# Kernel optimization log

Measured on AMD Instinct MI355X. Metric: run time of the kernel, lower is better.

## Reference

```python
import jax, jax.numpy as jnp
import numpy as np

# static 3D multi-scale configuration (transoar-style)
SS = np.array([[24, 24, 24], [12, 12, 12], [6, 6, 6], [3, 3, 3]], dtype=np.int64)  # (D,H,W) per level
NPL = SS.prod(1)
LSI = np.concatenate([[0], np.cumsum(NPL)[:-1]]).astype(np.int64)
S = int(NPL.sum())  # 15795 flattened tokens
B, C, HH, L, P = 2, 256, 8, 4, 4
DH = C // HH
NQ, FF = 80, 1024
NENC, NDEC = 6, 6
EPS = 1e-5


def layer_norm(x, g, b):
    mu = jnp.mean(x, -1, keepdims=True)
    var = jnp.mean((x - mu) ** 2, -1, keepdims=True)
    return (x - mu) * jax.lax.rsqrt(var + EPS) * g + b


def mha(q, k, v, in_w, in_b, out_w, out_b, mask=None):
    # torch nn.MultiheadAttention math (batch-first layout here)
    wq, wk, wv = jnp.split(in_w, 3, 0)
    bq, bk, bv = jnp.split(in_b, 3, 0)
    qh = (q @ wq.T + bq).reshape(B, -1, HH, DH)
    kh = (k @ wk.T + bk).reshape(B, -1, HH, DH)
    vh = (v @ wv.T + bv).reshape(B, -1, HH, DH)
    logits = jnp.einsum('bqhd,bkhd->bhqk', qh, kh) / jnp.float32(np.sqrt(DH))
    if mask is not None:  # bool mask, True = blocked
        logits = jnp.where(mask[None, None], jnp.float32(-1e9), logits)
    att = jax.nn.softmax(logits, -1)
    o = jnp.einsum('bhqk,bkhd->bqhd', att, vh).reshape(B, -1, C)
    return o @ out_w.T + out_b


def ms_deform_attn(query, ref, value_in, off_w, off_b, aw_w, aw_b, val_w, val_b, out_w, out_b):
    # 3D multi-scale deformable attention (deformable-DETR, trilinear sampling,
    # zero padding outside, align_corners=False semantics)
    Nq = query.shape[1]
    value = (value_in @ val_w.T + val_b).reshape(B, S, HH, DH)
    off = (query @ off_w.T + off_b).reshape(B, Nq, HH, L, P, 3)
    aw = jax.nn.softmax((query @ aw_w.T + aw_b).reshape(B, Nq, HH, L * P), -1)
    aw = aw.reshape(B, Nq, HH, L, P)
    norm = jnp.asarray(SS[:, ::-1].copy(), jnp.float32)  # (W,H,D) per level -> xyz order
    loc = ref[:, :, None, :, None, :] + off / norm[None, None, None, :, None, :]  # [B,Nq,HH,L,P,3]
    out = jnp.zeros((B, Nq, HH, DH), query.dtype)
    for lvl in range(L):
        D_, H_, W_ = (int(s) for s in SS[lvl])
        s0 = int(LSI[lvl])
        v = value[:, s0:s0 + D_ * H_ * W_].transpose(0, 2, 1, 3).reshape(B * HH, D_ * H_ * W_, DH)
        l = loc[:, :, :, lvl].transpose(0, 2, 1, 3, 4).reshape(B * HH, Nq * P, 3)
        x = l[..., 0] * W_ - 0.5
        y = l[..., 1] * H_ - 0.5
        z = l[..., 2] * D_ - 0.5
        x0, y0, z0 = jnp.floor(x), jnp.floor(y), jnp.floor(z)
        samp = jnp.zeros((B * HH, Nq * P, DH), query.dtype)
        for dz in (0, 1):
            for dy in (0, 1):
                for dx in (0, 1):
                    xi, yi, zi = x0 + dx, y0 + dy, z0 + dz
                    w = (1 - jnp.abs(x - xi)) * (1 - jnp.abs(y - yi)) * (1 - jnp.abs(z - zi))
                    ok = (xi >= 0) & (xi < W_) & (yi >= 0) & (yi < H_) & (zi >= 0) & (zi < D_)
                    idx = ((jnp.clip(zi, 0, D_ - 1) * H_ + jnp.clip(yi, 0, H_ - 1)) * W_
                           + jnp.clip(xi, 0, W_ - 1)).astype(jnp.int32)
                    samp = samp + jnp.take_along_axis(v, idx[..., None], axis=1) * (w * ok)[..., None]
        samp = samp.reshape(B, HH, Nq, P, DH)
        out = out + jnp.einsum('bhqpd,bhqp->bqhd', samp, aw[:, :, :, lvl].transpose(0, 2, 1, 3))
    return out.reshape(B, Nq, C) @ out_w.T + out_b


def get_reference_points(valid_ratios):
    refs = []
    for D_, H_, W_ in SS:
        z = (np.arange(D_) + 0.5) / D_
        y = (np.arange(H_) + 0.5) / H_
        x = (np.arange(W_) + 0.5) / W_
        zz, yy, xx = np.meshgrid(z, y, x, indexing='ij')
        refs.append(np.stack([xx.ravel(), yy.ravel(), zz.ravel()], -1))
    ref = jnp.asarray(np.concatenate(refs, 0).astype(np.float32))  # [S,3] xyz
    return ref[None, :, None, :] * valid_ratios[:, None]  # [B,S,L,3]


def _forward(fl, attn_mask):
    (src, pos, lvl_pos, tgt, query_pos, valid_ratios,
     eow, eob, eaw, eab, evw, evb, eouw, eoub, el1g, el1b, ef1w, ef1b, ef2w, ef2b, el2g, el2b,
     dsiw, dsib, dsow, dsob, dciw, dcib, dcow, dcob,
     dl1g, dl1b, dl2g, dl2b, dl3g, dl3b, df1w, df1b, df2w, df2b) = fl
    ref = get_reference_points(valid_ratios)
    out = src
    for i in range(NENC):
        a = ms_deform_attn(out + pos, ref, out, eow[i], eob[i], eaw[i], eab[i],
                           evw[i], evb[i], eouw[i], eoub[i])
        out = layer_norm(out + a, el1g[i], el1b[i])
        h = jax.nn.relu(out @ ef1w[i].T + ef1b[i])
        out = layer_norm(out + h @ ef2w[i].T + ef2b[i], el2g[i], el2b[i])
    memory = out
    q = tgt
    for i in range(NDEC):
        qk = q + query_pos
        sa = mha(qk, qk, q, dsiw[i], dsib[i], dsow[i], dsob[i])
        q = layer_norm(q + sa, dl2g[i], dl2b[i])
        ca = mha(q + query_pos, memory + lvl_pos, memory, dciw[i], dcib[i], dcow[i], dcob[i],
                 mask=attn_mask)
        q = layer_norm(q + ca, dl1g[i], dl1b[i])
        h = jax.nn.relu(q @ df1w[i].T + df1b[i])
        q = layer_norm(q + h @ df2w[i].T + df2b[i], dl3g[i], dl3b[i])
    return q


def setup_inputs() -> dict:
    key = jax.random.key(0)
    it = iter(jax.random.split(key, 64))
    def nrm(shape, s=0.02):
        return jax.random.normal(next(it), shape, jnp.float32) * s
    HLPO, HLP = HH * L * P * 3, HH * L * P
    inp = {}
    inp['src'] = nrm((B, S, C), 1.0)
    inp['pos'] = nrm((B, S, C), 1.0)
    inp['lvl_pos'] = nrm((B, S, C), 1.0)
    inp['tgt'] = nrm((B, NQ, C), 1.0)
    inp['query_pos'] = nrm((B, NQ, C), 1.0)
    inp['valid_ratios'] = jnp.ones((B, L, 3), jnp.float32)
    inp['enc_off_w'] = nrm((NENC, HLPO, C))
    inp['enc_off_b'] = nrm((NENC, HLPO), 0.1)
    inp['enc_aw_w'] = nrm((NENC, HLP, C))
    inp['enc_aw_b'] = jnp.zeros((NENC, HLP), jnp.float32)
    inp['enc_val_w'] = nrm((NENC, C, C))
    inp['enc_val_b'] = jnp.zeros((NENC, C), jnp.float32)
    inp['enc_out_w'] = nrm((NENC, C, C))
    inp['enc_out_b'] = jnp.zeros((NENC, C), jnp.float32)
    inp['enc_ln1_g'] = jnp.ones((NENC, C), jnp.float32)
    inp['enc_ln1_b'] = jnp.zeros((NENC, C), jnp.float32)
    inp['enc_fc1_w'] = nrm((NENC, FF, C))
    inp['enc_fc1_b'] = jnp.zeros((NENC, FF), jnp.float32)
    inp['enc_fc2_w'] = nrm((NENC, C, FF))
    inp['enc_fc2_b'] = jnp.zeros((NENC, C), jnp.float32)
    inp['enc_ln2_g'] = jnp.ones((NENC, C), jnp.float32)
    inp['enc_ln2_b'] = jnp.zeros((NENC, C), jnp.float32)
    inp['dec_sa_in_w'] = nrm((NDEC, 3 * C, C))
    inp['dec_sa_in_b'] = jnp.zeros((NDEC, 3 * C), jnp.float32)
    inp['dec_sa_out_w'] = nrm((NDEC, C, C))
    inp['dec_sa_out_b'] = jnp.zeros((NDEC, C), jnp.float32)
    inp['dec_ca_in_w'] = nrm((NDEC, 3 * C, C))
    inp['dec_ca_in_b'] = jnp.zeros((NDEC, 3 * C), jnp.float32)
    inp['dec_ca_out_w'] = nrm((NDEC, C, C))
    inp['dec_ca_out_b'] = jnp.zeros((NDEC, C), jnp.float32)
    inp['dec_ln1_g'] = jnp.ones((NDEC, C), jnp.float32)
    inp['dec_ln1_b'] = jnp.zeros((NDEC, C), jnp.float32)
    inp['dec_ln2_g'] = jnp.ones((NDEC, C), jnp.float32)
    inp['dec_ln2_b'] = jnp.zeros((NDEC, C), jnp.float32)
    inp['dec_ln3_g'] = jnp.ones((NDEC, C), jnp.float32)
    inp['dec_ln3_b'] = jnp.zeros((NDEC, C), jnp.float32)
    inp['dec_fc1_w'] = nrm((NDEC, FF, C))
    inp['dec_fc1_b'] = jnp.zeros((NDEC, FF), jnp.float32)
    inp['dec_fc2_w'] = nrm((NDEC, C, FF))
    inp['dec_fc2_b'] = jnp.zeros((NDEC, C), jnp.float32)
    inp['attn_mask'] = jax.random.bernoulli(next(it), 0.5, (NQ, S))
    inp['spatial_shapes'] = jnp.asarray(SS, jnp.int32)
    inp['level_start_index'] = jnp.asarray(LSI, jnp.int32)
    return inp


def reference(src, pos, lvl_pos, tgt, query_pos, valid_ratios,
              enc_off_w, enc_off_b, enc_aw_w, enc_aw_b, enc_val_w, enc_val_b, enc_out_w, enc_out_b,
              enc_ln1_g, enc_ln1_b, enc_fc1_w, enc_fc1_b, enc_fc2_w, enc_fc2_b, enc_ln2_g, enc_ln2_b,
              dec_sa_in_w, dec_sa_in_b, dec_sa_out_w, dec_sa_out_b,
              dec_ca_in_w, dec_ca_in_b, dec_ca_out_w, dec_ca_out_b,
              dec_ln1_g, dec_ln1_b, dec_ln2_g, dec_ln2_b, dec_ln3_g, dec_ln3_b,
              dec_fc1_w, dec_fc1_b, dec_fc2_w, dec_fc2_b,
              attn_mask, spatial_shapes, level_start_index):
    fl = (src, pos, lvl_pos, tgt, query_pos, valid_ratios,
          enc_off_w, enc_off_b, enc_aw_w, enc_aw_b, enc_val_w, enc_val_b, enc_out_w, enc_out_b,
          enc_ln1_g, enc_ln1_b, enc_fc1_w, enc_fc1_b, enc_fc2_w, enc_fc2_b, enc_ln2_g, enc_ln2_b,
          dec_sa_in_w, dec_sa_in_b, dec_sa_out_w, dec_sa_out_b,
          dec_ca_in_w, dec_ca_in_b, dec_ca_out_w, dec_ca_out_b,
          dec_ln1_g, dec_ln1_b, dec_ln2_g, dec_ln2_b, dec_ln3_g, dec_ln3_b,
          dec_fc1_w, dec_fc1_b, dec_fc2_w, dec_fc2_b)
    return _forward(fl, attn_mask)
```

## Files before the change

### kernel.cpp

```cpp
#include <hip/hip_runtime.h>
#include <cstdint>

#define S_TOT 15795
#define B_SZ 2
#define NQ 80
#define XSPLIT 128
#define NSPLIT 124
#define XCHUNK 128
#define MP 31616

typedef __attribute__((ext_vector_type(8))) short short8;
typedef __attribute__((ext_vector_type(4))) float f32x4;
typedef __attribute__((ext_vector_type(2))) float f32x2;

__device__ __forceinline__ unsigned short f2bf(float f) {
    unsigned u = __float_as_uint(f);
    unsigned r = u + 0x7fffu + ((u >> 16) & 1u);
    return (unsigned short)(r >> 16);
}

__global__ __launch_bounds__(256)
void cast_bf16_kernel(const float* __restrict__ x, unsigned short* __restrict__ o, int n4)
{
    int i = blockIdx.x * 256 + threadIdx.x;
    if (i < n4) {
        float4 v = ((const float4*)x)[i];
        ushort4 r;
        r.x = f2bf(v.x); r.y = f2bf(v.y); r.z = f2bf(v.z); r.w = f2bf(v.w);
        ((ushort4*)o)[i] = r;
    }
}

__global__ __launch_bounds__(256)
void init_enc_kernel(const float* __restrict__ src, const float* __restrict__ pos,
                     float* __restrict__ f_out, unsigned short* __restrict__ b_out,
                     unsigned short* __restrict__ b_mlp, int n4)
{
    int i = blockIdx.x * 256 + threadIdx.x;
    if (i < n4) {
        float4 s = ((const float4*)src)[i];
        float4 p = ((const float4*)pos)[i];
        ((float4*)f_out)[i] = s;
        ushort4 r, m;
        r.x = f2bf(s.x); r.y = f2bf(s.y); r.z = f2bf(s.z); r.w = f2bf(s.w);
        m.x = f2bf(s.x + p.x); m.y = f2bf(s.y + p.y);
        m.z = f2bf(s.z + p.z); m.w = f2bf(s.w + p.w);
        ((ushort4*)b_out)[i] = r;
        ((ushort4*)b_mlp)[i] = m;
    }
}

__global__ __launch_bounds__(256)
void cast_fuse_w_kernel(const float* __restrict__ eow, const float* __restrict__ eaw,
                        unsigned short* __restrict__ o)
{
    int i = blockIdx.x * 256 + threadIdx.x;
    const int n4 = 6 * 512 * 256 / 4;
    if (i < n4) {
        int e = i * 4;
        int layer = e / (512 * 256);
        int rem = e - layer * 512 * 256;
        int row = rem >> 8, col = rem & 255;
        const float* src = (row < 384)
            ? eow + ((size_t)layer * 384 + row) * 256 + col
            : eaw + ((size_t)layer * 128 + (row - 384)) * 256 + col;
        float4 v = *(const float4*)src;
        ushort4 r;
        r.x = f2bf(v.x); r.y = f2bf(v.y); r.z = f2bf(v.z); r.w = f2bf(v.w);
        ((ushort4*)o)[i] = r;
    }
}

__global__ __launch_bounds__(512)
void fuse_bias_kernel(const float* __restrict__ eob, const float* __restrict__ eab,
                      float* __restrict__ o)
{
    int i = blockIdx.x, t = threadIdx.x;
    o[i * 512 + t] = (t < 384) ? eob[i * 384 + t] : eab[i * 128 + (t - 384)];
}

__global__ __launch_bounds__(256)
void mask_pack_kernel(const unsigned char* __restrict__ mask,
                      unsigned long long* __restrict__ mp, int Lk)
{
    __shared__ unsigned char ml[80][260];
    const int k0 = blockIdx.x * 256;
    const int t = threadIdx.x;
    for (int idx = t; idx < 80 * 256; idx += 256) {
        int q = idx >> 8, kk = idx & 255;
        int kg = k0 + kk;
        ml[q][kk] = (kg < Lk) ? mask[(size_t)q * Lk + kg] : 1;
    }
    __syncthreads();
    int kg = k0 + t;
    if (kg < Lk) {
        unsigned long long lo = 0, hi = 0;
        #pragma unroll
        for (int q = 0; q < 64; ++q)
            lo |= (unsigned long long)(ml[q][t] ? 1u : 0u) << q;
        #pragma unroll
        for (int q = 0; q < 16; ++q)
            hi |= (unsigned long long)(ml[64 + q][t] ? 1u : 0u) << q;
        mp[2 * kg] = lo; mp[2 * kg + 1] = hi;
    }
}

__global__ __launch_bounds__(256)
void gemm_bf16_kernel(const unsigned short* __restrict__ A,
                      const unsigned short* __restrict__ B,
                      const float* __restrict__ bias, void* __restrict__ Yv,
                      int M, int N, int K, int mode)
{
    __shared__ unsigned short As[2][128 * 32];
    __shared__ unsigned short Bs[2][128 * 32];
    const int t = threadIdx.x;
    const int wave = t >> 6, lane = t & 63;
    const int quad = lane >> 4, l16 = lane & 15;
    const int bm0 = blockIdx.y * 128;
    const int bn0 = blockIdx.x * 128;
    const int wm = (wave & 1) * 64;
    const int wn = (wave >> 1) * 64;
    const int srow = t >> 2;
    const int scol = (t & 3) * 8;

    f32x4 acc[4][4] = {};

    const unsigned short* pa0 = A + (size_t)(bm0 + srow) * K + scol;
    const unsigned short* pa1 = pa0 + (size_t)64 * K;
    const unsigned short* pb0 = B + (size_t)(bn0 + srow) * K + scol;
    const unsigned short* pb1 = pb0 + (size_t)64 * K;

    #define GLL(src, dst)                                                        \
        __builtin_amdgcn_global_load_lds(                                        \
            (const __attribute__((address_space(1))) unsigned int*)(const void*)(src), \
            (__attribute__((address_space(3))) unsigned int*)(void*)(dst),       \
            16, 0, 0)

    const int nk = K / 32;
    GLL(pa0, &As[0][wave * 512]);
    GLL(pa1, &As[0][2048 + wave * 512]);
    GLL(pb0, &Bs[0][wave * 512]);
    GLL(pb1, &Bs[0][2048 + wave * 512]);
    __syncthreads();

    for (int kb = 0; kb < nk; ++kb) {
        const int cur = kb & 1, nxt = cur ^ 1;
        if (kb + 1 < nk) {
            const int k0 = (kb + 1) * 32;
            GLL(pa0 + k0, &As[nxt][wave * 512]);
            GLL(pa1 + k0, &As[nxt][2048 + wave * 512]);
            GLL(pb0 + k0, &Bs[nxt][wave * 512]);
            GLL(pb1 + k0, &Bs[nxt][2048 + wave * 512]);
        }

        short8 af[4], bf[4];
        #pragma unroll
        for (int im = 0; im < 4; ++im)
            af[im] = *(const short8*)&As[cur][(wm + im * 16 + l16) * 32 + quad * 8];
        #pragma unroll
        for (int in = 0; in < 4; ++in)
            bf[in] = *(const short8*)&Bs[cur][(wn + in * 16 + l16) * 32 + quad * 8];
        #pragma unroll
        for (int im = 0; im < 4; ++im)
            #pragma unroll
            for (int in = 0; in < 4; ++in)
                acc[im][in] = __builtin_amdgcn_mfma_f32_16x16x32_bf16(
                    bf[in], af[im], acc[im][in], 0, 0, 0);

        __syncthreads();
    }
    #undef GLL

    #pragma unroll
    for (int im = 0; im < 4; ++im) {
        const int gm = bm0 + wm + im * 16 + l16;
        if (gm >= M) continue;
        #pragma unroll
        for (int in = 0; in < 4; ++in) {
            const int gn0 = bn0 + wn + in * 16 + quad * 4;
            const float4 bv = *(const float4*)(bias + gn0);
            float o0 = acc[im][in][0] + bv.x;
            float o1 = acc[im][in][1] + bv.y;
            float o2 = acc[im][in][2] + bv.z;
            float o3 = acc[im][in][3] + bv.w;
            if (mode == 1) {
                o0 = fmaxf(o0, 0.f); o1 = fmaxf(o1, 0.f);
                o2 = fmaxf(o2, 0.f); o3 = fmaxf(o3, 0.f);
            }
            if (mode == 0) {
                float4 o = make_float4(o0, o1, o2, o3);
                *(float4*)((float*)Yv + (size_t)gm * N + gn0) = o;
            } else {
                ushort4 r4;
                r4.x = f2bf(o0); r4.y = f2bf(o1);
                r4.z = f2bf(o2); r4.w = f2bf(o3);
                *(ushort4*)((unsigned short*)Yv + (size_t)gm * N + gn0) = r4;
            }
        }
    }
}

__global__ __launch_bounds__(256)
void gemm_bias_kernel(const float* __restrict__ X, const float* __restrict__ Xadd,
                      const float* __restrict__ W,
                      const float* __restrict__ bias, float* __restrict__ Y,
                      int M, int N, int K, int relu)
{
    __shared__ float Xs[16][68];
    __shared__ float Ws[16][68];
    const int bm0 = blockIdx.y * 64;
    const int bn0 = blockIdx.x * 64;
    const int t = threadIdx.x;
    const int tx = t & 15, ty = t >> 4;
    const int lr = t >> 2;
    const int lk = (t & 3) << 2;
    float acc[4][4] = {};
    const int xr = bm0 + lr;
    const int wr = bn0 + lr;
    const float* xp = X + (size_t)xr * K + lk;
    const float* xap = Xadd ? Xadd + (size_t)xr * K + lk : nullptr;
    const float* wp = W + (size_t)wr * K + lk;
    for (int k0 = 0; k0 < K; k0 += 16) {
        float4 xv = make_float4(0.f, 0.f, 0.f, 0.f);
        if (xr < M) {
            xv = *(const float4*)(xp + k0);
            if (xap) {
                float4 av = *(const float4*)(xap + k0);
                xv.x += av.x; xv.y += av.y; xv.z += av.z; xv.w += av.w;
            }
        }
        float4 wv = make_float4(0.f, 0.f, 0.f, 0.f);
        if (wr < N) wv = *(const float4*)(wp + k0);
        Xs[lk + 0][lr] = xv.x; Xs[lk + 1][lr] = xv.y;
        Xs[lk + 2][lr] = xv.z; Xs[lk + 3][lr] = xv.w;
        Ws[lk + 0][lr] = wv.x; Ws[lk + 1][lr] = wv.y;
        Ws[lk + 2][lr] = wv.z; Ws[lk + 3][lr] = wv.w;
        __syncthreads();
        #pragma unroll
        for (int k = 0; k < 16; ++k) {
            float a0 = Xs[k][ty * 4 + 0], a1 = Xs[k][ty * 4 + 1];
            float a2 = Xs[k][ty * 4 + 2], a3 = Xs[k][ty * 4 + 3];
            float b0 = Ws[k][tx * 4 + 0], b1 = Ws[k][tx * 4 + 1];
            float b2 = Ws[k][tx * 4 + 2], b3 = Ws[k][tx * 4 + 3];
            acc[0][0] += a0 * b0; acc[0][1] += a0 * b1; acc[0][2] += a0 * b2; acc[0][3] += a0 * b3;
            acc[1][0] += a1 * b0; acc[1][1] += a1 * b1; acc[1][2] += a1 * b2; acc[1][3] += a1 * b3;
            acc[2][0] += a2 * b0; acc[2][1] += a2 * b1; acc[2][2] += a2 * b2; acc[2][3] += a2 * b3;
            acc[3][0] += a3 * b0; acc[3][1] += a3 * b1; acc[3][2] += a3 * b2; acc[3][3] += a3 * b3;
        }
        __syncthreads();
    }
    const int c0 = bn0 + tx * 4;
    float4 bv = *(const float4*)(bias + c0);
    #pragma unroll
    for (int i = 0; i < 4; ++i) {
        int r = bm0 + ty * 4 + i;
        if (r >= M) continue;
        float4 o;
        o.x = acc[i][0] + bv.x; o.y = acc[i][1] + bv.y;
        o.z = acc[i][2] + bv.z; o.w = acc[i][3] + bv.w;
        if (relu) {
            o.x = fmaxf(o.x, 0.f); o.y = fmaxf(o.y, 0.f);
            o.z = fmaxf(o.z, 0.f); o.w = fmaxf(o.w, 0.f);
        }
        *(float4*)(Y + (size_t)r * N + c0) = o;
    }
}

__global__ __launch_bounds__(256)
void ln_res_kernel(const float* __restrict__ X, const float* __restrict__ R,
                   const float* __restrict__ g, const float* __restrict__ bta,
                   float* __restrict__ O, unsigned short* __restrict__ Ob,
                   const float* __restrict__ Padd, unsigned short* __restrict__ Oadd,
                   int nrows)
{
    const int row = blockIdx.x * 4 + (threadIdx.x >> 6);
    if (row >= nrows) return;
    const int t = threadIdx.x & 63;
    const float4 xv = ((const float4*)(X + (size_t)row * 256))[t];
    const float4 rv = ((const float4*)(R + (size_t)row * 256))[t];
    float v0 = xv.x + rv.x, v1 = xv.y + rv.y, v2 = xv.z + rv.z, v3 = xv.w + rv.w;
    float s = v0 + v1 + v2 + v3;
    #pragma unroll
    for (int off = 32; off >= 1; off >>= 1) s += __shfl_xor(s, off, 64);
    float mu = s * (1.f / 256.f);
    float d0 = v0 - mu, d1 = v1 - mu, d2 = v2 - mu, d3 = v3 - mu;
    float s2 = d0 * d0 + d1 * d1 + d2 * d2 + d3 * d3;
    #pragma unroll
    for (int off = 32; off >= 1; off >>= 1) s2 += __shfl_xor(s2, off, 64);
    float rstd = rsqrtf(s2 * (1.f / 256.f) + 1e-5f);
    const float4 gv = ((const float4*)g)[t];
    const float4 bv = ((const float4*)bta)[t];
    float o0 = d0 * rstd * gv.x + bv.x;
    float o1 = d1 * rstd * gv.y + bv.y;
    float o2 = d2 * rstd * gv.z + bv.z;
    float o3 = d3 * rstd * gv.w + bv.w;
    ((float4*)(O + (size_t)row * 256))[t] = make_float4(o0, o1, o2, o3);
    if (Ob) {
        ushort4 r4;
        r4.x = f2bf(o0); r4.y = f2bf(o1); r4.z = f2bf(o2); r4.w = f2bf(o3);
        ((ushort4*)(Ob + (size_t)row * 256))[t] = r4;
    }
    if (Oadd) {
        const float4 pv = ((const float4*)(Padd + (size_t)row * 256))[t];
        ushort4 r4;
        r4.x = f2bf(o0 + pv.x); r4.y = f2bf(o1 + pv.y);
        r4.z = f2bf(o2 + pv.z); r4.w = f2bf(o3 + pv.w);
        ((ushort4*)(Oadd + (size_t)row * 256))[t] = r4;
    }
}

__global__ __launch_bounds__(256)
void deform_kernel(const float* __restrict__ offaw,
                   const unsigned short* __restrict__ value,
                   unsigned short* __restrict__ out)
{
    const int nwg = B_SZ * S_TOT;
    const int qq = nwg >> 3, rr = nwg & 7;
    const int xcd = blockIdx.x & 7, chunk_off = blockIdx.x >> 3;
    const int bq = (xcd < rr ? xcd * (qq + 1) : rr * (qq + 1) + (xcd - rr) * qq) + chunk_off;
    const int b = bq / S_TOT;
    const int s = bq - b * S_TOT;
    const int t = threadIdx.x;

    __shared__ float2 tbl[128][9];

    if (t < 128) {
        const int h = t >> 4, lp = t & 15, l = lp >> 2;
        float logit = offaw[(size_t)bq * 512 + 384 + t];
        float m = logit;
        m = fmaxf(m, __shfl_xor(m, 1, 64));
        m = fmaxf(m, __shfl_xor(m, 2, 64));
        m = fmaxf(m, __shfl_xor(m, 4, 64));
        m = fmaxf(m, __shfl_xor(m, 8, 64));
        float e = __expf(logit - m);
        float su = e;
        su += __shfl_xor(su, 1, 64);
        su += __shfl_xor(su, 2, 64);
        su += __shfl_xor(su, 4, 64);
        su += __shfl_xor(su, 8, 64);
        float aw = e / su;

        int iz, iy, ix; float invn;
        if (s < 13824)      { invn = 1.f / 24.f; int tl = s;
                              iz = tl / 576; int r1 = tl - iz * 576;
                              iy = r1 / 24;  ix = r1 - iy * 24; }
        else if (s < 15552) { invn = 1.f / 12.f; int tl = s - 13824;
                              iz = tl / 144; int r1 = tl - iz * 144;
                              iy = r1 / 12;  ix = r1 - iy * 12; }
        else if (s < 15768) { invn = 1.f / 6.f;  int tl = s - 15552;
                              iz = tl / 36;  int r1 = tl - iz * 36;
                              iy = r1 / 6;   ix = r1 - iy * 6; }
        else                { invn = 1.f / 3.f;  int tl = s - 15768;
                              iz = tl / 9;   int r1 = tl - iz * 9;
                              iy = r1 / 3;   ix = r1 - iy * 3; }
        float rx = (ix + 0.5f) * invn;
        float ry = (iy + 0.5f) * invn;
        float rz = (iz + 0.5f) * invn;

        const int lvl_n[4]  = {24, 12, 6, 3};
        const int lvl_s0[4] = {0, 13824, 15552, 15768};
        const int nl = lvl_n[l];
        const int s0l = lvl_s0[l];
        const float* op = offaw + (size_t)bq * 512 + t * 3;
        float x = rx * nl + op[0] - 0.5f;
        float y = ry * nl + op[1] - 0.5f;
        float z = rz * nl + op[2] - 0.5f;
        float fx = floorf(x), fy = floorf(y), fz = floorf(z);
        int x0 = (int)fx, y0 = (int)fy, z0 = (int)fz;
        float wx1 = x - fx, wx0 = 1.f - wx1;
        float wy1 = y - fy, wy0 = 1.f - wy1;
        float wz1 = z - fz, wz0 = 1.f - wz1;
        int xc0 = min(max(x0, 0), nl - 1), xc1 = min(max(x0 + 1, 0), nl - 1);
        int yc0 = min(max(y0, 0), nl - 1), yc1 = min(max(y0 + 1, 0), nl - 1);
        int zc0 = min(max(z0, 0), nl - 1), zc1 = min(max(z0 + 1, 0), nl - 1);
        bool ox0 = (x0 >= 0) && (x0 < nl);
        bool ox1 = (x0 + 1 >= 0) && (x0 + 1 < nl);
        bool oy0 = (y0 >= 0) && (y0 < nl), oy1 = (y0 + 1 >= 0) && (y0 + 1 < nl);
        bool oz0 = (z0 >= 0) && (z0 < nl), oz1 = (z0 + 1 >= 0) && (z0 + 1 < nl);
        int base = b * S_TOT + s0l;
        #pragma unroll
        for (int c = 0; c < 8; ++c) {
            int dx = c & 1, dy = (c >> 1) & 1, dz = c >> 2;
            float w = (dx ? wx1 : wx0) * (dy ? wy1 : wy0) * (dz ? wz1 : wz0);
            bool ok = (dx ? ox1 : ox0) && (dy ? oy1 : oy0) && (dz ? oz1 : oz0);
            int xi = dx ? xc1 : xc0;
            int yi = dy ? yc1 : yc0;
            int zi = dz ? zc1 : zc0;
            int elem = ((base + (zi * nl + yi) * nl + xi) * 8 + h) << 6;
            tbl[t][c] = make_float2(ok ? w * aw : 0.f, __int_as_float(elem));
        }
    }
    __syncthreads();

    const int c16 = t & 3, z = t >> 2, cr = z & 7, h = z >> 3;
    const float2* trow = &tbl[h * 16][cr];
    const unsigned cofs = (unsigned)(c16 * 16);
    f32x2 a01 = {0.f, 0.f}, a23 = {0.f, 0.f}, a45 = {0.f, 0.f}, a67 = {0.f, 0.f};
    #pragma unroll
    for (int p = 0; p < 16; ++p) {
        float2 e = trow[p * 9];
        unsigned off = __float_as_uint(e.y) + cofs;
        const uint4 dv = *(const uint4*)((const char*)value + off);
        f32x2 w2 = {e.x, e.x};
        f32x2 v01 = {__uint_as_float(dv.x << 16), __uint_as_float(dv.x & 0xffff0000u)};
        f32x2 v23 = {__uint_as_float(dv.y << 16), __uint_as_float(dv.y & 0xffff0000u)};
        f32x2 v45 = {__uint_as_float(dv.z << 16), __uint_as_float(dv.z & 0xffff0000u)};
        f32x2 v67 = {__uint_as_float(dv.w << 16), __uint_as_float(dv.w & 0xffff0000u)};
        asm("v_pk_fma_f32 %0, %1, %2, %0" : "+v"(a01) : "v"(v01), "v"(w2));
        asm("v_pk_fma_f32 %0, %1, %2, %0" : "+v"(a23) : "v"(v23), "v"(w2));
        asm("v_pk_fma_f32 %0, %1, %2, %0" : "+v"(a45) : "v"(v45), "v"(w2));
        asm("v_pk_fma_f32 %0, %1, %2, %0" : "+v"(a67) : "v"(v67), "v"(w2));
    }
    float acc[8] = {a01.x, a01.y, a23.x, a23.y, a45.x, a45.y, a67.x, a67.y};
    #pragma unroll
    for (int i = 0; i < 8; ++i) {
        acc[i] += __shfl_xor(acc[i], 4, 64);
        acc[i] += __shfl_xor(acc[i], 8, 64);
        acc[i] += __shfl_xor(acc[i], 16, 64);
    }
    if ((t & 28) == 0) {
        uint4 r;
        r.x = (unsigned)f2bf(acc[0]) | ((unsigned)f2bf(acc[1]) << 16);
        r.y = (unsigned)f2bf(acc[2]) | ((unsigned)f2bf(acc[3]) << 16);
        r.z = (unsigned)f2bf(acc[4]) | ((unsigned)f2bf(acc[5]) << 16);
        r.w = (unsigned)f2bf(acc[6]) | ((unsigned)f2bf(acc[7]) << 16);
        *(uint4*)(out + (size_t)bq * 256 + h * 32 + c16 * 8) = r;
    }
}

__global__ __launch_bounds__(256)
void attn_kernel(const float* __restrict__ Q, const float* __restrict__ K,
                 const float* __restrict__ V, float* __restrict__ O,
                 int Lq, int Lk, float scale, int ldq, int ldk)
{
    const int nqc = (Lq + 3) >> 2;
    const int blk = blockIdx.x;
    const int qc = blk % nqc;
    const int bh = blk / nqc;
    const int h = bh & 7;
    const int b = bh >> 3;
    const int qi0 = qc * 4;
    const int t = threadIdx.x;
    const int c = t & 31, g = t >> 5;

    float qv[4];
    #pragma unroll
    for (int j = 0; j < 4; ++j)
        qv[j] = Q[((size_t)(b * Lq + qi0 + j)) * ldq + h * 32 + c];

    float m[4], l[4], acc[4];
    #pragma unroll
    for (int j = 0; j < 4; ++j) { m[j] = -1e30f; l[j] = 0.f; acc[j] = 0.f; }

    for (int k = g; k < Lk; k += 8) {
        float kv = K[((size_t)(b * Lk + k)) * ldk + h * 32 + c];
        float vv = V[((size_t)(b * Lk + k)) * 256 + h * 32 + c];
        #pragma unroll
        for (int j = 0; j < 4; ++j) {
            float p = qv[j] * kv;
            p += __shfl_xor(p, 16, 32);
            p += __shfl_xor(p, 8, 32);
            p += __shfl_xor(p, 4, 32);
            p += __shfl_xor(p, 2, 32);
            p += __shfl_xor(p, 1, 32);
            float sc = p * scale;
            float mn = fmaxf(m[j], sc);
            float fo = __expf(m[j] - mn);
            float w = __expf(sc - mn);
            l[j] = l[j] * fo + w;
            acc[j] = acc[j] * fo + w * vv;
            m[j] = mn;
        }
    }
    __shared__ float sm[8][4], sl[8][4], sacc[8][4][32];
    if (c == 0) {
        #pragma unroll
        for (int j = 0; j < 4; ++j) { sm[g][j] = m[j]; sl[g][j] = l[j]; }
    }
    #pragma unroll
    for (int j = 0; j < 4; ++j) sacc[g][j][c] = acc[j];
    __syncthreads();
    if (g == 0) {
        #pragma unroll
        for (int j = 0; j < 4; ++j) {
            float M = -1e30f;
            #pragma unroll
            for (int i = 0; i < 8; ++i) M = fmaxf(M, sm[i][j]);
            float L = 0.f, o = 0.f;
            #pragma unroll
            for (int i = 0; i < 8; ++i) {
                float e = __expf(sm[i][j] - M);
                L += sl[i][j] * e;
                o += sacc[i][j][c] * e;
            }
            O[((size_t)(b * Lq + qi0 + j)) * 256 + h * 32 + c] = o / L;
        }
    }
}

__global__ __launch_bounds__(320)
void xattn_part_kernel(const float* __restrict__ Q,
                       const unsigned short* __restrict__ K,
                       const unsigned short* __restrict__ V,
                       const unsigned long long* __restrict__ mp,
                       float* __restrict__ pm, float* __restrict__ pl,
                       float* __restrict__ po, int Lk, float scale)
{
    const int split = blockIdx.x;
    const int bh = blockIdx.y;
    const int b = bh >> 3, h = bh & 7;
    const int t = threadIdx.x;
    const int wave = t >> 6, lane = t & 63;
    const int l16 = lane & 15, quad = lane >> 4;

    __shared__ unsigned short Ks[128][40];
    __shared__ unsigned short Vt[32][136];
    __shared__ unsigned short Ps[80][40];
    __shared__ unsigned long long Mw[2][128];

    const int k_base = split * XCHUNK;

    for (int idx = t; idx < 512; idx += 320) {
        int key = idx >> 2, cg = (idx & 3) * 8;
        int kg = k_base + key;
        short8 kv = {0, 0, 0, 0, 0, 0, 0, 0};
        short8 vv = {0, 0, 0, 0, 0, 0, 0, 0};
        if (kg < Lk) {
            size_t go = ((size_t)(b * Lk + kg)) * 256 + h * 32 + cg;
            kv = *(const short8*)(K + go);
            vv = *(const short8*)(V + go);
        }
        *(short8*)&Ks[key][cg] = kv;
        #pragma unroll
        for (int j = 0; j < 8; ++j)
            Vt[cg + j][key] = (unsigned short)vv[j];
    }
    if (t < 128) {
        int kg = k_base + t;
        unsigned long long lo = ~0ULL, hi = ~0ULL;
        if (kg < Lk) { lo = mp[2 * kg]; hi = mp[2 * kg + 1]; }
        Mw[0][t] = lo; Mw[1][t] = hi;
    }

    const int q = wave * 16 + l16;
    short8 qf;
    {
        const float* qp = Q + ((size_t)(b * NQ + q)) * 256 + h * 32 + quad * 8;
        float4 q0 = *(const float4*)qp;
        float4 q1 = *(const float4*)(qp + 4);
        unsigned short* qh = (unsigned short*)&qf;
        qh[0] = f2bf(q0.x * scale); qh[1] = f2bf(q0.y * scale);
        qh[2] = f2bf(q0.z * scale); qh[3] = f2bf(q0.w * scale);
        qh[4] = f2bf(q1.x * scale); qh[5] = f2bf(q1.y * scale);
        qh[6] = f2bf(q1.z * scale); qh[7] = f2bf(q1.w * scale);
    }
    __syncthreads();

    f32x4 sfr[8];
    const f32x4 zz = {0.f, 0.f, 0.f, 0.f};
    #pragma unroll
    for (int tt = 0; tt < 8; ++tt) {
        short8 kf = *(const short8*)&Ks[tt * 16 + l16][quad * 8];
        sfr[tt] = __builtin_amdgcn_mfma_f32_16x16x32_bf16(kf, qf, zz, 0, 0, 0);
    }

    const unsigned long long* mrow = Mw[wave >> 2];
    const int qbit = (wave < 4 ? wave * 16 : 0) + l16;
    const int widx = qbit >> 5;
    const int sh = qbit & 31;

    float sc[8][4];
    #pragma unroll
    for (int tt = 0; tt < 8; ++tt) {
        int k0 = tt * 16 + quad * 4;
        uint4 ma = *(const uint4*)&mrow[k0];
        uint4 mb = *(const uint4*)&mrow[k0 + 2];
        unsigned w0 = widx ? ma.y : ma.x;
        unsigned w1 = widx ? ma.w : ma.z;
        unsigned w2 = widx ? mb.y : mb.x;
        unsigned w3 = widx ? mb.w : mb.z;
        sc[tt][0] = ((w0 >> sh) & 1u) ? -1e9f : sfr[tt][0];
        sc[tt][1] = ((w1 >> sh) & 1u) ? -1e9f : sfr[tt][1];
        sc[tt][2] = ((w2 >> sh) & 1u) ? -1e9f : sfr[tt][2];
        sc[tt][3] = ((w3 >> sh) & 1u) ? -1e9f : sfr[tt][3];
    }
    float mx = -1e30f;
    #pragma unroll
    for (int tt = 0; tt < 8; ++tt)
        #pragma unroll
        for (int r = 0; r < 4; ++r) mx = fmaxf(mx, sc[tt][r]);
    mx = fmaxf(mx, __shfl_xor(mx, 16, 64));
    mx = fmaxf(mx, __shfl_xor(mx, 32, 64));
    float sum = 0.f;
    #pragma unroll
    for (int tt = 0; tt < 8; ++tt)
        #pragma unroll
        for (int r = 0; r < 4; ++r) {
            sc[tt][r] = __expf(sc[tt][r] - mx);
            sum += sc[tt][r];
        }
    sum += __shfl_xor(sum, 16, 64);
    sum += __shfl_xor(sum, 32, 64);

    f32x4 oacc[2] = {zz, zz};
    #pragma unroll
    for (int s = 0; s < 4; ++s) {
        #pragma unroll
        for (int tt = 0; tt < 2; ++tt) {
            int T = s * 2 + tt;
            unsigned plo = (unsigned)f2bf(sc[T][0]) | ((unsigned)f2bf(sc[T][1]) << 16);
            unsigned phi = (unsigned)f2bf(sc[T][2]) | ((unsigned)f2bf(sc[T][3]) << 16);
            unsigned* dst = (unsigned*)&Ps[q][tt * 16 + quad * 4];
            dst[0] = plo; dst[1] = phi;
        }
        asm volatile("" ::: "memory");
        short8 pf = *(const short8*)&Ps[q][quad * 8];
        short8 vf0 = *(const short8*)&Vt[l16][s * 32 + quad * 8];
        short8 vf1 = *(const short8*)&Vt[16 + l16][s * 32 + quad * 8];
        oacc[0] = __builtin_amdgcn_mfma_f32_16x16x32_bf16(vf0, pf, oacc[0], 0, 0, 0);
        oacc[1] = __builtin_amdgcn_mfma_f32_16x16x32_bf16(vf1, pf, oacc[1], 0, 0, 0);
    }

    const size_t obase = ((size_t)bh * NSPLIT + split) * NQ;
    #pragma unroll
    for (int c = 0; c < 2; ++c)
        #pragma unroll
        for (int r = 0; r < 4; ++r)
            po[(obase + q) * 32 + c * 16 + quad * 4 + r] = oacc[c][r];
    if (quad == 0) { pm[obase + q] = mx; pl[obase + q] = sum; }
}

__global__ __launch_bounds__(64)
void xattn_merge_kernel(const float* __restrict__ pm, const float* __restrict__ pl,
                        const float* __restrict__ po, float* __restrict__ O)
{
    const int idx = blockIdx.x;
    const int bh = idx / NQ, q = idx - bh * NQ;
    const int b = bh >> 3, h = bh & 7;
    const int tt = threadIdx.x;
    if (tt >= 32) return;
    const int c = tt;
    float M = -1e30f;
    for (int s = 0; s < NSPLIT; ++s)
        M = fmaxf(M, pm[((size_t)bh * NSPLIT + s) * NQ + q]);
    float L = 0.f, o = 0.f;
    for (int s = 0; s < NSPLIT; ++s) {
        size_t base = ((size_t)bh * NSPLIT + s) * NQ + q;
        float e = __expf(pm[base] - M);
        L += pl[base] * e;
        o += po[base * 32 + c] * e;
    }
    O[((size_t)(b * NQ + q)) * 256 + h * 32 + c] = o / L;
}

extern "C" void kernel_launch(void* const* d_in, const int* in_sizes, int n_in,
                              void* d_out, int out_size, void* d_ws, size_t ws_size,
                              hipStream_t stream)
{
    const float* src       = (const float*)d_in[0];
    const float* pos       = (const float*)d_in[1];
    const float* lvl_pos   = (const float*)d_in[2];
    const float* tgt       = (const float*)d_in[3];
    const float* query_pos = (const float*)d_in[4];
    const float* eow  = (const float*)d_in[6];
    const float* eob  = (const float*)d_in[7];
    const float* eaw  = (const float*)d_in[8];
    const float* eab  = (const float*)d_in[9];
    const float* evw  = (const float*)d_in[10];
    const float* evb  = (const float*)d_in[11];
    const float* eouw = (const float*)d_in[12];
    const float* eoub = (const float*)d_in[13];
    const float* el1g = (const float*)d_in[14];
    const float* el1b = (const float*)d_in[15];
    const float* ef1w = (const float*)d_in[16];
    const float* ef1b = (const float*)d_in[17];
    const float* ef2w = (const float*)d_in[18];
    const float* ef2b = (const float*)d_in[19];
    const float* el2g = (const float*)d_in[20];
    const float* el2b = (const float*)d_in[21];
    const float* dsiw = (const float*)d_in[22];
    const float* dsib = (const float*)d_in[23];
    const float* dsow = (const float*)d_in[24];
    const float* dsob = (const float*)d_in[25];
    const float* dciw = (const float*)d_in[26];
    const float* dcib = (const float*)d_in[27];
    const float* dcow = (const float*)d_in[28];
    const float* dcob = (const float*)d_in[29];
    const float* dl1g = (const float*)d_in[30];
    const float* dl1b = (const float*)d_in[31];
    const float* dl2g = (const float*)d_in[32];
    const float* dl2b = (const float*)d_in[33];
    const float* dl3g = (const float*)d_in[34];
    const float* dl3b = (const float*)d_in[35];
    const float* df1w = (const float*)d_in[36];
    const float* df1b = (const float*)d_in[37];
    const float* df2w = (const float*)d_in[38];
    const float* df2b = (const float*)d_in[39];
    const unsigned char* amask = (const unsigned char*)d_in[40];

    const int MBS = B_SZ * S_TOT;
    const size_t nBSC = (size_t)MBS * 256;
    const size_t nP   = (size_t)MP * 256;
    const size_t nFFA = (size_t)MBS * 512 + 16384;

    float* ws = (float*)d_ws;
    float* f_out = ws; ws += nP;
    float* f_mlp = ws; ws += nP;
    float* f_ffa = ws; ws += nFFA;
    float* f_offaw = f_ffa;
    float* f_val = ws; ws += nP;
    float* d_q   = ws; ws += 40960;
    float* d_qkp = ws; ws += 81920;
    float* d_sq  = ws; ws += 40960;
    float* d_sv  = ws; ws += 40960;
    float* d_ao  = ws; ws += 40960;
    float* d_pr  = ws; ws += 40960;
    float* d_h   = ws; ws += 163840;
    float* x_pm  = ws; ws += (size_t)16 * XSPLIT * NQ;
    float* x_pl  = ws; ws += (size_t)16 * XSPLIT * NQ;
    float* x_po  = ws; ws += (size_t)16 * XSPLIT * NQ * 32;
    unsigned long long* x_mp = (unsigned long long*)ws; ws += 2 * 16384;
    float* f_fb  = ws; ws += 6 * 512;

    unsigned short* bws = (unsigned short*)ws;
    unsigned short* b_mlp  = bws; bws += nP;
    unsigned short* b_out  = bws; bws += nP;
    unsigned short* w_eoaw = bws; bws += (size_t)6 * 512 * 256;
    unsigned short* w_evw  = bws; bws += (size_t)6 * 256 * 256;
    unsigned short* w_eouw = bws; bws += (size_t)6 * 256 * 256;
    unsigned short* w_ef1  = bws; bws += (size_t)6 * 1024 * 256;
    unsigned short* w_ef2  = bws; bws += (size_t)6 * 256 * 1024;
    unsigned short* w_dciw = bws; bws += (size_t)6 * 768 * 256;

    unsigned short* b_hs   = (unsigned short*)f_ffa;
    unsigned short* b_samp = b_mlp;
    unsigned short* b_val  = (unsigned short*)x_pm;
    unsigned short* b_xk   = (unsigned short*)f_offaw;
    unsigned short* b_xv   = (unsigned short*)f_val;

    auto gemmb = [&](const unsigned short* A, const unsigned short* W, const float* bb,
                     void* Y, int M, int N, int K, int mode) {
        dim3 grid(N / 128, (M + 127) / 128);
        gemm_bf16_kernel<<<grid, dim3(256), 0, stream>>>(A, W, bb, Y, M, N, K, mode);
    };
    auto gemms = [&](const float* X, const float* Xadd, const float* W, const float* bb,
                     float* Y, int M, int N, int K, int relu) {
        dim3 grid(N / 64, (M + 63) / 64);
        gemm_bias_kernel<<<grid, dim3(256), 0, stream>>>(X, Xadd, W, bb, Y, M, N, K, relu);
    };
    auto cast = [&](const float* x, unsigned short* o, size_t n) {
        int n4c = (int)(n / 4);
        cast_bf16_kernel<<<(n4c + 255) / 256, 256, 0, stream>>>(x, o, n4c);
    };

    const int n4 = (int)(nBSC / 4);
    const float scale = 0.17677669529663687f;
    const int lnGrid = (MBS + 3) / 4;

    {
        const int nf4 = 6 * 512 * 256 / 4;
        cast_fuse_w_kernel<<<(nf4 + 255) / 256, 256, 0, stream>>>(eow, eaw, w_eoaw);
        fuse_bias_kernel<<<6, 512, 0, stream>>>(eob, eab, f_fb);
        mask_pack_kernel<<<(S_TOT + 255) / 256, 256, 0, stream>>>(amask, x_mp, S_TOT);
    }
    cast(evw,  w_evw,  (size_t)6 * 256 * 256);
    cast(eouw, w_eouw, (size_t)6 * 256 * 256);
    cast(ef1w, w_ef1,  (size_t)6 * 1024 * 256);
    cast(ef2w, w_ef2,  (size_t)6 * 256 * 1024);
    cast(dciw, w_dciw, (size_t)6 * 768 * 256);

    init_enc_kernel<<<(n4 + 255) / 256, 256, 0, stream>>>(src, pos, f_out, b_out, b_mlp, n4);

    for (int i = 0; i < 6; ++i) {
        gemmb(b_mlp, w_eoaw + (size_t)i * 512 * 256, f_fb + i * 512, f_offaw, MBS, 512, 256, 0);
        gemmb(b_out, w_evw + (size_t)i * 256 * 256, evb + i * 256, b_val, MBS, 256, 256, 2);
        deform_kernel<<<MBS, 256, 0, stream>>>(f_offaw, b_val, b_samp);
        gemmb(b_samp, w_eouw + (size_t)i * 256 * 256, eoub + i * 256, f_mlp, MBS, 256, 256, 0);
        ln_res_kernel<<<lnGrid, 256, 0, stream>>>(f_out, f_mlp, el1g + i * 256, el1b + i * 256,
                                                  f_out, b_out, (const float*)nullptr,
                                                  (unsigned short*)nullptr, MBS);
        gemmb(b_out, w_ef1 + (size_t)i * 1024 * 256, ef1b + i * 1024, b_hs, MBS, 1024, 256, 1);
        gemmb(b_hs, w_ef2 + (size_t)i * 256 * 1024, ef2b + i * 256, f_val, MBS, 256, 1024, 0);
        ln_res_kernel<<<lnGrid, 256, 0, stream>>>(f_out, f_val, el2g + i * 256, el2b + i * 256,
                                                  f_out, b_out, (i < 5 ? pos : lvl_pos),
                                                  b_mlp, MBS);
    }

    hipMemcpyAsync(d_q, tgt, 40960 * sizeof(float), hipMemcpyDeviceToDevice, stream);

    for (int i = 0; i < 6; ++i) {
        const float* siw = dsiw + (size_t)i * 768 * 256;
        const float* sib = dsib + (size_t)i * 768;
        gemms(d_q, query_pos, siw, sib, d_qkp, 160, 512, 256, 0);
        gemms(d_q, nullptr, siw + 512 * 256, sib + 512, d_sv, 160, 256, 256, 0);
        attn_kernel<<<B_SZ * 8 * (NQ / 4), 256, 0, stream>>>(
            d_qkp, d_qkp + 256, d_sv, d_ao, NQ, NQ, scale, 512, 512);
        gemms(d_ao, nullptr, dsow + (size_t)i * 256 * 256, dsob + i * 256, d_pr, 160, 256, 256, 0);
        ln_res_kernel<<<40, 256, 0, stream>>>(d_q, d_pr, dl2g + i * 256, dl2b + i * 256,
                                              d_q, (unsigned short*)nullptr,
                                              (const float*)nullptr, (unsigned short*)nullptr, 160);

        const float* cib = dcib + (size_t)i * 768;
        gemms(d_q, query_pos, dciw + (size_t)i * 768 * 256, cib, d_sq, 160, 256, 256, 0);
        gemmb(b_mlp, w_dciw + (size_t)i * 768 * 256 + 256 * 256, cib + 256,
              b_xk, MBS, 256, 256, 2);
        gemmb(b_out, w_dciw + (size_t)i * 768 * 256 + 512 * 256, cib + 512,
              b_xv, MBS, 256, 256, 2);
        xattn_part_kernel<<<dim3(NSPLIT, 16), 320, 0, stream>>>(
            d_sq, b_xk, b_xv, x_mp, x_pm, x_pl, x_po, S_TOT, scale);
        xattn_merge_kernel<<<16 * NQ, 64, 0, stream>>>(x_pm, x_pl, x_po, d_ao);
        gemms(d_ao, nullptr, dcow + (size_t)i * 256 * 256, dcob + i * 256, d_pr, 160, 256, 256, 0);
        ln_res_kernel<<<40, 256, 0, stream>>>(d_q, d_pr, dl1g + i * 256, dl1b + i * 256,
                                              d_q, (unsigned short*)nullptr,
                                              (const float*)nullptr, (unsigned short*)nullptr, 160);

        gemms(d_q, nullptr, df1w + (size_t)i * 1024 * 256, df1b + i * 1024, d_h, 160, 1024, 256, 1);
        gemms(d_h, nullptr, df2w + (size_t)i * 256 * 1024, df2b + i * 256, d_pr, 160, 256, 1024, 0);
        ln_res_kernel<<<40, 256, 0, stream>>>(d_q, d_pr, dl3g + i * 256, dl3b + i * 256,
                                              d_q, (unsigned short*)nullptr,
                                              (const float*)nullptr, (unsigned short*)nullptr, 160);
    }

    hipMemcpyAsync(d_out, d_q, 40960 * sizeof(float), hipMemcpyDeviceToDevice, stream);
}
```

Measured before the change: 3.709 ms.

## Fuse encoder output projections with residual add and LayerNorm in one GEMM kernel

Adds a bf16 MFMA GEMM kernel where each block computes full 256-wide rows (64 rows per block), then adds bias and the residual and applies LayerNorm in registers. It writes fp32 and bf16 outputs and, optionally, a bf16 copy with the positional embedding added. This replaces the separate out-proj/FFN2 GEMMs and ln_res kernels in the encoder, removing an fp32 intermediate round trip through memory and extra launches. The trade-off is a smaller grid (M/64 blocks) and 64 accumulator vectors per thread, which may lower occupancy for the K=1024 FFN GEMM.

Measured after the change: 3.653 ms. Within noise of the previous version (-1.5%).

```diff
diff --git a/kernel.cpp b/kernel.cpp
--- a/kernel.cpp
+++ b/kernel.cpp
@@ -196,6 +196,114 @@
                 r4.z = f2bf(o2); r4.w = f2bf(o3);
                 *(ushort4*)((unsigned short*)Yv + (size_t)gm * N + gn0) = r4;
             }
+        }
+    }
+}
+
+__global__ __launch_bounds__(256)
+void gemm_ln_kernel(const unsigned short* __restrict__ A,
+                    const unsigned short* __restrict__ B,
+                    const float* __restrict__ bias,
+                    const float* __restrict__ g, const float* __restrict__ bta,
+                    float* __restrict__ Fout, unsigned short* __restrict__ Bout,
+                    const float* __restrict__ Padd, unsigned short* __restrict__ Oadd,
+                    int M, int K)
+{
+    __shared__ unsigned short As[2][64 * 32];
+    __shared__ unsigned short Bs[2][256 * 32];
+    const int t = threadIdx.x;
+    const int wave = t >> 6, lane = t & 63;
+    const int quad = lane >> 4, l16 = lane & 15;
+    const int bm0 = blockIdx.x * 64;
+
+    f32x4 acc[16] = {};
+
+    const int srow4 = lane >> 2;
+    const int scol = (lane & 3) * 8;
+    const unsigned short* pa = A + (size_t)(bm0 + wave * 16 + srow4) * K + scol;
+    const unsigned short* pb = B + (size_t)(wave * 64 + srow4) * K + scol;
+
+    #define GLL(src, dst)                                                        \
+        __builtin_amdgcn_global_load_lds(                                        \
+            (const __attribute__((address_space(1))) unsigned int*)(const void*)(src), \
+            (__attribute__((address_space(3))) unsigned int*)(void*)(dst),       \
+            16, 0, 0)
+
+    const int nk = K / 32;
+    GLL(pa, (char*)As[0] + wave * 1024);
+    #pragma unroll
+    for (int j = 0; j < 4; ++j)
+        GLL(pb + (size_t)j * 16 * K, (char*)Bs[0] + (wave * 4 + j) * 1024);
+    __syncthreads();
+
+    for (int kb = 0; kb < nk; ++kb) {
+        const int cur = kb & 1, nxt = cur ^ 1;
+        if (kb + 1 < nk) {
+            const int k0 = (kb + 1) * 32;
+            GLL(pa + k0, (char*)As[nxt] + wave * 1024);
+            #pragma unroll
+            for (int j = 0; j < 4; ++j)
+                GLL(pb + (size_t)j * 16 * K + k0, (char*)Bs[nxt] + (wave * 4 + j) * 1024);
+        }
+
+        short8 af = *(const short8*)&As[cur][(wave * 16 + l16) * 32 + quad * 8];
+        #pragma unroll
+        for (int in = 0; in < 16; ++in) {
+            short8 bf = *(const short8*)&Bs[cur][(in * 16 + l16) * 32 + quad * 8];
+            acc[in] = __builtin_amdgcn_mfma_f32_16x16x32_bf16(bf, af, acc[in], 0, 0, 0);
+        }
+        __syncthreads();
+    }
+    #undef GLL
+
+    const int row = bm0 + wave * 16 + l16;
+    if (row >= M) return;
+
+    float s = 0.f;
+    #pragma unroll
+    for (int in = 0; in < 16; ++in) {
+        const int c0 = in * 16 + quad * 4;
+        const float4 bv = *(const float4*)(bias + c0);
+        const float4 rv = *(const float4*)(Fout + (size_t)row * 256 + c0);
+        acc[in][0] += bv.x + rv.x;
+        acc[in][1] += bv.y + rv.y;
+        acc[in][2] += bv.z + rv.z;
+        acc[in][3] += bv.w + rv.w;
+        s += acc[in][0] + acc[in][1] + acc[in][2] + acc[in][3];
+    }
+    s += __shfl_xor(s, 16, 64);
+    s += __shfl_xor(s, 32, 64);
+    const float mu = s * (1.f / 256.f);
+    float s2 = 0.f;
+    #pragma unroll
+    for (int in = 0; in < 16; ++in) {
+        float d0 = acc[in][0] - mu, d1 = acc[in][1] - mu;
+        float d2 = acc[in][2] - mu, d3 = acc[in][3] - mu;
+        s2 += d0 * d0 + d1 * d1 + d2 * d2 + d3 * d3;
+    }
+    s2 += __shfl_xor(s2, 16, 64);
+    s2 += __shfl_xor(s2, 32, 64);
+    const float rstd = rsqrtf(s2 * (1.f / 256.f) + 1e-5f);
+
+    #pragma unroll
+    for (int in = 0; in < 16; ++in) {
+        const int c0 = in * 16 + quad * 4;
+        const float4 gv = *(const float4*)(g + c0);
+        const float4 bt = *(const float4*)(bta + c0);
+        float o0 = (acc[in][0] - mu) * rstd * gv.x + bt.x;
+        float o1 = (acc[in][1] - mu) * rstd * gv.y + bt.y;
+        float o2 = (acc[in][2] - mu) * rstd * gv.z + bt.z;
+        float o3 = (acc[in][3] - mu) * rstd * gv.w + bt.w;
+        *(float4*)(Fout + (size_t)row * 256 + c0) = make_float4(o0, o1, o2, o3);
+        ushort4 r4;
+        r4.x = f2bf(o0); r4.y = f2bf(o1); r4.z = f2bf(o2); r4.w = f2bf(o3);
+        *(ushort4*)(Bout + (size_t)row * 256 + c0) = r4;
+        if (Oadd) {
+            const float4 pv = *(const float4*)(Padd + (size_t)row * 256 + c0);
+            ushort4 a4;
+            a4.x = f2bf(o0 + pv.x); a4.y = f2bf(o1 + pv.y);
+            a4.z = f2bf(o2 + pv.z); a4.w = f2bf(o3 + pv.w);
+            *(ushort4*)(Oadd + (size_t)row * 256 + c0) = a4;
         }
     }
 }
@@ -743,6 +851,12 @@
         dim3 grid(N / 128, (M + 127) / 128);
         gemm_bf16_kernel<<<grid, dim3(256), 0, stream>>>(A, W, bb, Y, M, N, K, mode);
     };
+    auto gemmln = [&](const unsigned short* A, const unsigned short* W, const float* bb,
+                      const float* lg, const float* lb, const float* padd,
+                      unsigned short* oadd, int M, int K) {
+        gemm_ln_kernel<<<(M + 63) / 64, dim3(256), 0, stream>>>(
+            A, W, bb, lg, lb, f_out, b_out, padd, oadd, M, K);
+    };
     auto gemms = [&](const float* X, const float* Xadd, const float* W, const float* bb,
                      float* Y, int M, int N, int K, int relu) {
         dim3 grid(N / 64, (M + 63) / 64);
@@ -755,7 +869,6 @@
 
     const int n4 = (int)(nBSC / 4);
     const float scale = 0.17677669529663687f;
-    const int lnGrid = (MBS + 3) / 4;
 
     {
         const int nf4 = 6 * 512 * 256 / 4;
@@ -775,15 +888,11 @@
         gemmb(b_mlp, w_eoaw + (size_t)i * 512 * 256, f_fb + i * 512, f_offaw, MBS, 512, 256, 0);
         gemmb(b_out, w_evw + (size_t)i * 256 * 256, evb + i * 256, b_val, MBS, 256, 256, 2);
         deform_kernel<<<MBS, 256, 0, stream>>>(f_offaw, b_val, b_samp);
-        gemmb(b_samp, w_eouw + (size_t)i * 256 * 256, eoub + i * 256, f_mlp, MBS, 256, 256, 0);
-        ln_res_kernel<<<lnGrid, 256, 0, stream>>>(f_out, f_mlp, el1g + i * 256, el1b + i * 256,
-                                                  f_out, b_out, (const float*)nullptr,
-                                                  (unsigned short*)nullptr, MBS);
+        gemmln(b_samp, w_eouw + (size_t)i * 256 * 256, eoub + i * 256,
+               el1g + i * 256, el1b + i * 256, nullptr, nullptr, MBS, 256);
         gemmb(b_out, w_ef1 + (size_t)i * 1024 * 256, ef1b + i * 1024, b_hs, MBS, 1024, 256, 1);
-        gemmb(b_hs, w_ef2 + (size_t)i * 256 * 1024, ef2b + i * 256, f_val, MBS, 256, 1024, 0);
-        ln_res_kernel<<<lnGrid, 256, 0, stream>>>(f_out, f_val, el2g + i * 256, el2b + i * 256,
-                                                  f_out, b_out, (i < 5 ? pos : lvl_pos),
-                                                  b_mlp, MBS);
+        gemmln(b_hs, w_ef2 + (size_t)i * 256 * 1024, ef2b + i * 256,
+               el2g + i * 256, el2b + i * 256, (i < 5 ? pos : lvl_pos), b_mlp, MBS, 1024);
     }
 
     hipMemcpyAsync(d_q, tgt, 40960 * sizeof(float), hipMemcpyDeviceToDevice, stream);
```
